# Kernel tuning notes

Hardware: AMD Instinct MI355X
Metric: run time of the kernel (lower is better)

## Reference

```python
import jax, jax.numpy as jnp
import numpy as np

T, B, D, H = 512, 64, 1024, 1024


def setup_inputs() -> dict:
    key = jax.random.key(0)
    ks = jax.random.split(key, 6)
    s_in = 0.02  # small init so tanh/sigmoid don't saturate
    return {
        "x": jax.random.normal(ks[0], (T, B, D), jnp.float32),
        "Wih": jax.random.normal(ks[1], (D, 4 * H), jnp.float32) * s_in,
        "Whh": jax.random.normal(ks[2], (H, 4 * H), jnp.float32) * s_in,
        "b": jnp.zeros((4 * H,), jnp.float32),
        "Wih_r": jax.random.normal(ks[3], (D, 4 * H), jnp.float32) * s_in,
        "Whh_r": jax.random.normal(ks[4], (H, 4 * H), jnp.float32) * s_in,
        "b_r": jnp.zeros((4 * H,), jnp.float32),
    }


def _lstm_scan(x, Wih, Whh, b):
    """Run an LSTM over time-major x [T,B,D]; returns (hs [T,B,H], h_T, c_T)."""
    Bsz = x.shape[1]
    h0 = jnp.zeros((Bsz, H), x.dtype)
    c0 = jnp.zeros((Bsz, H), x.dtype)

    # Precompute input projections for all timesteps in one big GEMM.
    xg = jnp.einsum("tbd,dg->tbg", x, Wih) + b  # [T,B,4H]

    def step(carry, xg_t):
        h, c = carry
        gates = xg_t + h @ Whh  # [B,4H]
        i, f, g, o = jnp.split(gates, 4, axis=-1)
        c_next = jax.nn.sigmoid(f) * c + jax.nn.sigmoid(i) * jnp.tanh(g)
        h_next = jax.nn.sigmoid(o) * jnp.tanh(c_next)
        return (h_next, c_next), h_next

    (hT, cT), hs = jax.lax.scan(step, (h0, c0), xg)
    return hs, hT, cT


def reference(x, Wih, Whh, b, Wih_r, Whh_r, b_r):
    # forward direction
    hs_f, hT, cT = _lstm_scan(x, Wih, Whh, b)
    # backward direction: flip time, run, flip outputs back
    hs_b, _, _ = _lstm_scan(x[::-1], Wih_r, Whh_r, b_r)
    output = jnp.concatenate([hs_f, hs_b[::-1]], axis=-1)  # [T,B,2H]
    # original returns (output, h_n) where h_n is the forward cell's final (h, c)
    return output, hT, cT
```

## Files before the change

### kernel.cpp

```cpp
#include <hip/hip_runtime.h>
#include <hip/hip_bf16.h>


#define TS    512
#define BATCH 64
#define DDIM  1024
#define HDIM  1024
#define KD    2048
#define GD    4096
#define OUT_HS ((size_t)TS * BATCH * 2 * HDIM)
#define HT_OFF OUT_HS
#define CT_OFF (OUT_HS + (size_t)BATCH * HDIM)

#define WP_BYTES   ((size_t)2 * GD * KD * 2)
#define XBF_BYTES  ((size_t)TS * BATCH * DDIM * 2)
#define HS_BYTES   ((size_t)2 * 2 * BATCH * HDIM * 2)
#define BAR_BYTES  ((size_t)4096)
#define WS_A_TOTAL (WP_BYTES + XBF_BYTES + HS_BYTES + BAR_BYTES)
#define WS_B_TOTAL (WP_BYTES + HS_BYTES + BAR_BYTES)

typedef __attribute__((ext_vector_type(8))) short frag8;
typedef __attribute__((ext_vector_type(4))) float f32x4;
typedef unsigned long long u64;

__device__ __forceinline__ ushort f2b(float f) {
  union { float f; unsigned u; } v; v.f = f;
  unsigned r = v.u + 0x7FFFu + ((v.u >> 16) & 1u);
  return (ushort)(r >> 16);
}
__device__ __forceinline__ float sigf(float x) { return 1.0f / (1.0f + __expf(-x)); }
__device__ __forceinline__ float tanh_fast(float x) {
  x = fminf(15.0f, fmaxf(-15.0f, x));
  float e = __expf(2.0f * x);
  return (e - 1.0f) / (e + 1.0f);
}


__global__ void xconv(const float* __restrict__ x, ushort* __restrict__ o) {
  size_t i = ((size_t)blockIdx.x * 256 + threadIdx.x) * 8;
  float4 a = *(const float4*)(x + i);
  float4 b = *(const float4*)(x + i + 4);
  union { ushort s[8]; uint4 v; } r;
  r.s[0] = f2b(a.x); r.s[1] = f2b(a.y); r.s[2] = f2b(a.z); r.s[3] = f2b(a.w);
  r.s[4] = f2b(b.x); r.s[5] = f2b(b.y); r.s[6] = f2b(b.z); r.s[7] = f2b(b.w);
  *(uint4*)(o + i) = r.v;
}

__global__ void wpackk(const float* __restrict__ Wih,  const float* __restrict__ Whh,
                       const float* __restrict__ WihR, const float* __restrict__ WhhR,
                       ushort* __restrict__ wp) {
  __shared__ ushort tile[32][36];
  int bid = blockIdx.x;
  int kt  = bid & 63;
  int pt  = (bid >> 6) & 127;
  int dir = bid >> 13;
  const float* Wi = dir ? WihR : Wih;
  const float* Wh = dir ? WhhR : Whh;
  int t  = threadIdx.x;
  int kl = t >> 3;
  int g  = (t >> 1) & 3;
  int q  = t & 1;
  int k  = kt * 32 + kl;
  const float* srow = (k < 1024) ? (Wi + (size_t)k * GD) : (Wh + (size_t)(k - 1024) * GD);
  float4 v = *(const float4*)(srow + g * 1024 + pt * 8 + q * 4);
  int pl = g * 8 + q * 4;
  tile[kl][pl + 0] = f2b(v.x); tile[kl][pl + 1] = f2b(v.y);
  tile[kl][pl + 2] = f2b(v.z); tile[kl][pl + 3] = f2b(v.w);
  __syncthreads();
  int po = t >> 3;
  int kc = t & 7;
  ushort* dst = wp + ((size_t)dir * GD + pt * 32 + po) * KD + kt * 32 + kc * 4;
  ushort4 ov;
  ov.x = tile[kc * 4 + 0][po]; ov.y = tile[kc * 4 + 1][po];
  ov.z = tile[kc * 4 + 2][po]; ov.w = tile[kc * 4 + 3][po];
  *(ushort4*)dst = ov;
}

#define MFMA(a, b, c) __builtin_amdgcn_mfma_f32_16x16x32_bf16((a), (b), (c), 0, 0, 0)
#define ALOADU64(p) __hip_atomic_load((p), __ATOMIC_RELAXED, __HIP_MEMORY_SCOPE_AGENT)

template <int MODEA>
__global__ __launch_bounds__(256, 1)
void lstm_scan(const ushort* __restrict__ xbf, const float* __restrict__ xf,
               const ushort* __restrict__ wpack,
               const float* __restrict__ bfwd, const float* __restrict__ bbwd,
               ushort* hstate, float* __restrict__ out, unsigned* bar) {
  __shared__ ushort wlds[32 * KD];

  const int tid  = threadIdx.x;
  const int lane = tid & 63;
  const int wv   = tid >> 6;
  const int wg   = blockIdx.x;
  const int dir  = wg >> 7;
  const int wq   = wg & 127;
  unsigned* grpflags = bar + (dir * 4 + wv) * 128;

  {
    const ushort* src = wpack + ((size_t)dir * GD + wq * 32) * KD;
#pragma unroll
    for (int it = 0; it < 32; ++it) {
      int m  = it * 256 + tid;
      int p  = m >> 8;
      int kc = m & 255;
      uint4 v = *(const uint4*)(src + (size_t)p * KD + kc * 8);
      int off = p * 4096 + ((kc * 16) ^ ((p & 7) << 4));
      *(uint4*)((char*)wlds + off) = v;
    }
  }
  __syncthreads();

  const int lm   = lane & 15;
  const int jj   = lane & 7;
  const int kb   = (lane >> 4) * 8;
  const int kb2  = kb * 2;
  const int arow = wv * 16 + lm;
  const int hcol = wq * 8 + jj;
  const int sw   = jj << 4;
  const int b0base = lm * 4096;
  const int b1base = (16 + lm) * 4096;

  const float* bsrc = dir ? bbwd : bfwd;
  const float bias0 = bsrc[(lm >> 3) * HDIM + hcol];
  const float bias1 = bsrc[(2 + (lm >> 3)) * HDIM + hcol];

  float creg[4] = {0.f, 0.f, 0.f, 0.f};
  f32x4 a0a, a0b, a1a, a1b;

  auto compute_x = [&](int tt) {
    const int tsrc = dir ? (TS - 1 - tt) : tt;
    a0a = (f32x4){0.f,0.f,0.f,0.f}; a0b = (f32x4){0.f,0.f,0.f,0.f};
    a1a = (f32x4){0.f,0.f,0.f,0.f}; a1b = (f32x4){0.f,0.f,0.f,0.f};
    if (MODEA) {
      const ushort* xs = xbf + ((size_t)tsrc * BATCH + arow) * DDIM + kb;
#pragma unroll 8
      for (int kk = 0; kk < 32; kk += 2) {
        frag8 a  = *(const frag8*)(xs + kk * 32);
        frag8 a2 = *(const frag8*)(xs + (kk + 1) * 32);
        int ko  = (kk * 64 + kb2) ^ sw;
        int ko2 = ((kk + 1) * 64 + kb2) ^ sw;
        frag8 b0  = *(const frag8*)((const char*)wlds + (b0base + ko));
        frag8 b1  = *(const frag8*)((const char*)wlds + (b1base + ko));
        frag8 b02 = *(const frag8*)((const char*)wlds + (b0base + ko2));
        frag8 b12 = *(const frag8*)((const char*)wlds + (b1base + ko2));
        a0a = MFMA(a, b0, a0a);  a1a = MFMA(a, b1, a1a);
        a0b = MFMA(a2, b02, a0b); a1b = MFMA(a2, b12, a1b);
      }
    } else {
      const float* xs = xf + ((size_t)tsrc * BATCH + arow) * DDIM + kb;
#pragma unroll 4
      for (int kk = 0; kk < 32; ++kk) {
        float4 f0 = *(const float4*)(xs + kk * 32);
        float4 f1 = *(const float4*)(xs + kk * 32 + 4);
        union { ushort s[8]; frag8 fr; } ua;
        ua.s[0] = f2b(f0.x); ua.s[1] = f2b(f0.y); ua.s[2] = f2b(f0.z); ua.s[3] = f2b(f0.w);
        ua.s[4] = f2b(f1.x); ua.s[5] = f2b(f1.y); ua.s[6] = f2b(f1.z); ua.s[7] = f2b(f1.w);
        int ko = (kk * 64 + kb2) ^ sw;
        frag8 b0 = *(const frag8*)((const char*)wlds + (b0base + ko));
        frag8 b1 = *(const frag8*)((const char*)wlds + (b1base + ko));
        if (kk & 1) { a0b = MFMA(ua.fr, b0, a0b); a1b = MFMA(ua.fr, b1, a1b); }
        else        { a0a = MFMA(ua.fr, b0, a0a); a1a = MFMA(ua.fr, b1, a1a); }
      }
    }
  };

  auto h_part = [&](int t) {
    const ushort* hsrd = hstate + (((size_t)(t & 1) * 2 + dir) * BATCH + arow) * HDIM + kb;
    frag8 hf[32];
#pragma unroll
    for (int kk = 0; kk < 32; ++kk)
      asm volatile("global_load_dwordx4 %0, %1, off offset:%2 sc1"
                   : "=v"(hf[kk]) : "v"(hsrd), "i"(kk * 64) : "memory");
    asm volatile("s_waitcnt vmcnt(0)" ::: "memory");
    __builtin_amdgcn_sched_barrier(0);
#pragma unroll
    for (int kk = 0; kk < 32; kk += 2) {
      int ko  = (2048 + kk * 64 + kb2) ^ sw;
      int ko2 = (2048 + (kk + 1) * 64 + kb2) ^ sw;
      frag8 b0  = *(const frag8*)((const char*)wlds + (b0base + ko));
      frag8 b1  = *(const frag8*)((const char*)wlds + (b1base + ko));
      frag8 b02 = *(const frag8*)((const char*)wlds + (b0base + ko2));
      frag8 b12 = *(const frag8*)((const char*)wlds + (b1base + ko2));
      a0a = MFMA(hf[kk], b0, a0a);      a1a = MFMA(hf[kk], b1, a1a);
      a0b = MFMA(hf[kk + 1], b02, a0b); a1b = MFMA(hf[kk + 1], b12, a1b);
    }
  };

  compute_x(0);

  for (int t = 0; t < TS; ++t) {
    if (t > 0) h_part(t);

    const int tsrc = dir ? (TS - 1 - t) : t;
    f32x4 acc0 = a0a + a0b;
    f32x4 acc1 = a1a + a1b;

    ushort* hnext = hstate + ((size_t)(((t + 1) & 1) * 2 + dir) * BATCH) * HDIM;
    const size_t obase = ((size_t)tsrc * BATCH) * (2 * HDIM) + (size_t)dir * HDIM + hcol;
    const bool last = (t == TS - 1);
    const bool last_f = (dir == 0) && last;

#pragma unroll
    for (int i = 0; i < 4; ++i) {
      float g0 = acc0[i] + bias0;
      float g1 = acc1[i] + bias1;
      float q0 = __shfl_xor(g0, 8);
      float q1 = __shfl_xor(g1, 8);
      if ((lane & 8) == 0) {
        float cn = sigf(q0) * creg[i] + sigf(g0) * tanh_fast(g1);
        creg[i] = cn;
        float hv = sigf(q1) * tanh_fast(cn);
        int brow = wv * 16 + (lane >> 4) * 4 + i;
        out[obase + (size_t)brow * (2 * HDIM)] = hv;
        if (!last)
          __hip_atomic_store(hnext + (size_t)brow * HDIM + hcol, f2b(hv),
                             __ATOMIC_RELAXED, __HIP_MEMORY_SCOPE_AGENT);
        if (last_f) {
          out[HT_OFF + (size_t)brow * HDIM + hcol] = hv;
          out[CT_OFF + (size_t)brow * HDIM + hcol] = cn;
        }
      }
    }

    if (last) break;

    asm volatile("s_waitcnt vmcnt(0)" ::: "memory");
    if (lane == 0)
      __hip_atomic_store(grpflags + wq, (unsigned)(t + 1),
                         __ATOMIC_RELAXED, __HIP_MEMORY_SCOPE_AGENT);

    compute_x(t + 1);

    {
      const unsigned want = (unsigned)(t + 1);
      const u64* f2 = (const u64*)grpflags + lane;
      for (;;) {
        u64 v = ALOADU64(f2);
        if ((unsigned)v >= want && (unsigned)(v >> 32) >= want) break;
        __builtin_amdgcn_s_sleep(1);
      }
    }
    __atomic_signal_fence(__ATOMIC_SEQ_CST);
    asm volatile("" ::: "memory");
  }
}

extern "C" void kernel_launch(void* const* d_in, const int* in_sizes, int n_in,
                              void* d_out, int out_size, void* d_ws, size_t ws_size,
                              hipStream_t stream) {
  const float* x    = (const float*)d_in[0];
  const float* Wih  = (const float*)d_in[1];
  const float* Whh  = (const float*)d_in[2];
  const float* b    = (const float*)d_in[3];
  const float* WihR = (const float*)d_in[4];
  const float* WhhR = (const float*)d_in[5];
  const float* bR   = (const float*)d_in[6];
  float* out = (float*)d_out;
  char* ws = (char*)d_ws;

  if (ws_size < WS_B_TOTAL) return;
  const bool modeA = (ws_size >= WS_A_TOTAL);

  ushort* wp  = (ushort*)(ws);
  ushort* xbf = (ushort*)(ws + WP_BYTES);
  size_t hs_off = modeA ? (WP_BYTES + XBF_BYTES) : WP_BYTES;
  ushort* hs = (ushort*)(ws + hs_off);
  unsigned* bar = (unsigned*)(ws + hs_off + HS_BYTES);

  hipMemsetAsync(ws + hs_off + HS_BYTES, 0, BAR_BYTES, stream);

  wpackk<<<dim3(16384), dim3(256), 0, stream>>>(Wih, Whh, WihR, WhhR, wp);

  if (modeA) {
    xconv<<<dim3(16384), dim3(256), 0, stream>>>(x, xbf);
    lstm_scan<1><<<dim3(256), dim3(256), 0, stream>>>(xbf, x, wp, b, bR, hs, out, bar);
  } else {
    lstm_scan<0><<<dim3(256), dim3(256), 0, stream>>>(nullptr, x, wp, b, bR, hs, out, bar);
  }
}
```

Measured before the change: 4.585 ms.

## Move x-projection MFMAs after barrier poll to overlap with split h loads

In the bf16-input mode, the x-tile loads are issued before the grid-barrier poll, and their MFMAs are deferred until after it. The x MFMAs are then interleaved with the recurrent h loads, which are split into two halves with partial vmcnt waits so the MFMAs on the first half can start while the second half is still loading. The intent is to hide global-load latency on the recurrent critical path. In exchange, the x MFMAs now sit after the barrier and may lengthen each step, and holding 64 fragment registers at once raises register pressure.

```diff
diff --git a/kernel.cpp b/kernel.cpp
--- a/kernel.cpp
+++ b/kernel.cpp
@@ -78,6 +78,7 @@
 
 #define MFMA(a, b, c) __builtin_amdgcn_mfma_f32_16x16x32_bf16((a), (b), (c), 0, 0, 0)
 #define ALOADU64(p) __hip_atomic_load((p), __ATOMIC_RELAXED, __HIP_MEMORY_SCOPE_AGENT)
+#define SB() __builtin_amdgcn_sched_barrier(0)
 
 template <int MODEA>
 __global__ __launch_bounds__(256, 1)
@@ -125,80 +126,105 @@
 
   float creg[4] = {0.f, 0.f, 0.f, 0.f};
   f32x4 a0a, a0b, a1a, a1b;
-
-  auto compute_x = [&](int tt) {
+  frag8 xa[32];
+  frag8 hfA[16];
+  frag8 hfB[16];
+
+  auto xload_issue = [&](int tt) {
     const int tsrc = dir ? (TS - 1 - tt) : tt;
+    const ushort* xs = xbf + ((size_t)tsrc * BATCH + arow) * DDIM + kb;
+#pragma unroll
+    for (int kk = 0; kk < 32; ++kk)
+      asm volatile("global_load_dwordx4 %0, %1, off offset:%2"
+                   : "=v"(xa[kk]) : "v"(xs), "i"(kk * 64) : "memory");
+  };
+
+  auto x_mfma = [&]() {
     a0a = (f32x4){0.f,0.f,0.f,0.f}; a0b = (f32x4){0.f,0.f,0.f,0.f};
     a1a = (f32x4){0.f,0.f,0.f,0.f}; a1b = (f32x4){0.f,0.f,0.f,0.f};
-    if (MODEA) {
-      const ushort* xs = xbf + ((size_t)tsrc * BATCH + arow) * DDIM + kb;
-#pragma unroll 8
-      for (int kk = 0; kk < 32; kk += 2) {
-        frag8 a  = *(const frag8*)(xs + kk * 32);
-        frag8 a2 = *(const frag8*)(xs + (kk + 1) * 32);
-        int ko  = (kk * 64 + kb2) ^ sw;
-        int ko2 = ((kk + 1) * 64 + kb2) ^ sw;
-        frag8 b0  = *(const frag8*)((const char*)wlds + (b0base + ko));
-        frag8 b1  = *(const frag8*)((const char*)wlds + (b1base + ko));
-        frag8 b02 = *(const frag8*)((const char*)wlds + (b0base + ko2));
-        frag8 b12 = *(const frag8*)((const char*)wlds + (b1base + ko2));
-        a0a = MFMA(a, b0, a0a);  a1a = MFMA(a, b1, a1a);
-        a0b = MFMA(a2, b02, a0b); a1b = MFMA(a2, b12, a1b);
-      }
-    } else {
-      const float* xs = xf + ((size_t)tsrc * BATCH + arow) * DDIM + kb;
-#pragma unroll 4
-      for (int kk = 0; kk < 32; ++kk) {
-        float4 f0 = *(const float4*)(xs + kk * 32);
-        float4 f1 = *(const float4*)(xs + kk * 32 + 4);
-        union { ushort s[8]; frag8 fr; } ua;
-        ua.s[0] = f2b(f0.x); ua.s[1] = f2b(f0.y); ua.s[2] = f2b(f0.z); ua.s[3] = f2b(f0.w);
-        ua.s[4] = f2b(f1.x); ua.s[5] = f2b(f1.y); ua.s[6] = f2b(f1.z); ua.s[7] = f2b(f1.w);
-        int ko = (kk * 64 + kb2) ^ sw;
-        frag8 b0 = *(const frag8*)((const char*)wlds + (b0base + ko));
-        frag8 b1 = *(const frag8*)((const char*)wlds + (b1base + ko));
-        if (kk & 1) { a0b = MFMA(ua.fr, b0, a0b); a1b = MFMA(ua.fr, b1, a1b); }
-        else        { a0a = MFMA(ua.fr, b0, a0a); a1a = MFMA(ua.fr, b1, a1a); }
-      }
-    }
-  };
-
-  auto h_part = [&](int t) {
+#pragma unroll
+    for (int kk = 0; kk < 32; kk += 2) {
+      int ko  = (kk * 64 + kb2) ^ sw;
+      int ko2 = ((kk + 1) * 64 + kb2) ^ sw;
+      frag8 b0  = *(const frag8*)((const char*)wlds + (b0base + ko));
+      frag8 b1  = *(const frag8*)((const char*)wlds + (b1base + ko));
+      frag8 b02 = *(const frag8*)((const char*)wlds + (b0base + ko2));
+      frag8 b12 = *(const frag8*)((const char*)wlds + (b1base + ko2));
+      a0a = MFMA(xa[kk], b0, a0a);      a1a = MFMA(xa[kk], b1, a1a);
+      a0b = MFMA(xa[kk + 1], b02, a0b); a1b = MFMA(xa[kk + 1], b12, a1b);
+    }
+  };
+
+  auto hloadA = [&](int t) {
     const ushort* hsrd = hstate + (((size_t)(t & 1) * 2 + dir) * BATCH + arow) * HDIM + kb;
-    frag8 hf[32];
-#pragma unroll
-    for (int kk = 0; kk < 32; ++kk)
+#pragma unroll
+    for (int kk = 0; kk < 16; ++kk)
       asm volatile("global_load_dwordx4 %0, %1, off offset:%2 sc1"
-                   : "=v"(hf[kk]) : "v"(hsrd), "i"(kk * 64) : "memory");
-    asm volatile("s_waitcnt vmcnt(0)" ::: "memory");
-    __builtin_amdgcn_sched_barrier(0);
-#pragma unroll
-    for (int kk = 0; kk < 32; kk += 2) {
+                   : "=v"(hfA[kk]) : "v"(hsrd), "i"(kk * 64) : "memory");
+  };
+  auto hloadB = [&](int t) {
+    const ushort* hsrd = hstate + (((size_t)(t & 1) * 2 + dir) * BATCH + arow) * HDIM + kb;
+#pragma unroll
+    for (int kk = 0; kk < 16; ++kk)
+      asm volatile("global_load_dwordx4 %0, %1, off offset:%2 sc1"
+                   : "=v"(hfB[kk]) : "v"(hsrd), "i"(1024 + kk * 64) : "memory");
+  };
+
+  auto h_mfmaA = [&]() {
+#pragma unroll
+    for (int kk = 0; kk < 16; kk += 2) {
       int ko  = (2048 + kk * 64 + kb2) ^ sw;
       int ko2 = (2048 + (kk + 1) * 64 + kb2) ^ sw;
       frag8 b0  = *(const frag8*)((const char*)wlds + (b0base + ko));
       frag8 b1  = *(const frag8*)((const char*)wlds + (b1base + ko));
       frag8 b02 = *(const frag8*)((const char*)wlds + (b0base + ko2));
       frag8 b12 = *(const frag8*)((const char*)wlds + (b1base + ko2));
-      a0a = MFMA(hf[kk], b0, a0a);      a1a = MFMA(hf[kk], b1, a1a);
-      a0b = MFMA(hf[kk + 1], b02, a0b); a1b = MFMA(hf[kk + 1], b12, a1b);
-    }
-  };
-
-  compute_x(0);
-
-  for (int t = 0; t < TS; ++t) {
-    if (t > 0) h_part(t);
-
+      a0a = MFMA(hfA[kk], b0, a0a);      a1a = MFMA(hfA[kk], b1, a1a);
+      a0b = MFMA(hfA[kk + 1], b02, a0b); a1b = MFMA(hfA[kk + 1], b12, a1b);
+    }
+  };
+  auto h_mfmaB = [&]() {
+#pragma unroll
+    for (int kk = 16; kk < 32; kk += 2) {
+      int ko  = (2048 + kk * 64 + kb2) ^ sw;
+      int ko2 = (2048 + (kk + 1) * 64 + kb2) ^ sw;
+      frag8 b0  = *(const frag8*)((const char*)wlds + (b0base + ko));
+      frag8 b1  = *(const frag8*)((const char*)wlds + (b1base + ko));
+      frag8 b02 = *(const frag8*)((const char*)wlds + (b0base + ko2));
+      frag8 b12 = *(const frag8*)((const char*)wlds + (b1base + ko2));
+      a0a = MFMA(hfB[kk - 16], b0, a0a);      a1a = MFMA(hfB[kk - 16], b1, a1a);
+      a0b = MFMA(hfB[kk - 15], b02, a0b);     a1b = MFMA(hfB[kk - 15], b12, a1b);
+    }
+  };
+
+  auto compute_x_old = [&](int tt) {
+    const int tsrc = dir ? (TS - 1 - tt) : tt;
+    a0a = (f32x4){0.f,0.f,0.f,0.f}; a0b = (f32x4){0.f,0.f,0.f,0.f};
+    a1a = (f32x4){0.f,0.f,0.f,0.f}; a1b = (f32x4){0.f,0.f,0.f,0.f};
+    const float* xs = xf + ((size_t)tsrc * BATCH + arow) * DDIM + kb;
+#pragma unroll 4
+    for (int kk = 0; kk < 32; ++kk) {
+      float4 f0 = *(const float4*)(xs + kk * 32);
+      float4 f1 = *(const float4*)(xs + kk * 32 + 4);
+      union { ushort s[8]; frag8 fr; } ua;
+      ua.s[0] = f2b(f0.x); ua.s[1] = f2b(f0.y); ua.s[2] = f2b(f0.z); ua.s[3] = f2b(f0.w);
+      ua.s[4] = f2b(f1.x); ua.s[5] = f2b(f1.y); ua.s[6] = f2b(f1.z); ua.s[7] = f2b(f1.w);
+      int ko = (kk * 64 + kb2) ^ sw;
+      frag8 b0 = *(const frag8*)((const char*)wlds + (b0base + ko));
+      frag8 b1 = *(const frag8*)((const char*)wlds + (b1base + ko));
+      if (kk & 1) { a0b = MFMA(ua.fr, b0, a0b); a1b = MFMA(ua.fr, b1, a1b); }
+      else        { a0a = MFMA(ua.fr, b0, a0a); a1a = MFMA(ua.fr, b1, a1a); }
+    }
+  };
+
+  auto epilogue = [&](int t) {
     const int tsrc = dir ? (TS - 1 - t) : t;
     f32x4 acc0 = a0a + a0b;
     f32x4 acc1 = a1a + a1b;
-
     ushort* hnext = hstate + ((size_t)(((t + 1) & 1) * 2 + dir) * BATCH) * HDIM;
     const size_t obase = ((size_t)tsrc * BATCH) * (2 * HDIM) + (size_t)dir * HDIM + hcol;
     const bool last = (t == TS - 1);
     const bool last_f = (dir == 0) && last;
-
 #pragma unroll
     for (int i = 0; i < 4; ++i) {
       float g0 = acc0[i] + bias0;
@@ -220,27 +246,65 @@
         }
       }
     }
-
-    if (last) break;
-
+  };
+
+  auto publish = [&](int gen) {
     asm volatile("s_waitcnt vmcnt(0)" ::: "memory");
     if (lane == 0)
-      __hip_atomic_store(grpflags + wq, (unsigned)(t + 1),
+      __hip_atomic_store(grpflags + wq, (unsigned)gen,
                          __ATOMIC_RELAXED, __HIP_MEMORY_SCOPE_AGENT);
-
-    compute_x(t + 1);
-
-    {
-      const unsigned want = (unsigned)(t + 1);
-      const u64* f2 = (const u64*)grpflags + lane;
-      for (;;) {
-        u64 v = ALOADU64(f2);
-        if ((unsigned)v >= want && (unsigned)(v >> 32) >= want) break;
-        __builtin_amdgcn_s_sleep(1);
-      }
+  };
+
+  auto poll = [&](int gen) {
+    const unsigned want = (unsigned)gen;
+    const u64* f2 = (const u64*)grpflags + lane;
+    for (;;) {
+      u64 v = ALOADU64(f2);
+      if ((unsigned)v >= want && (unsigned)(v >> 32) >= want) break;
+      __builtin_amdgcn_s_sleep(1);
     }
     __atomic_signal_fence(__ATOMIC_SEQ_CST);
     asm volatile("" ::: "memory");
+  };
+
+  if (MODEA) {
+    xload_issue(0);
+    asm volatile("s_waitcnt vmcnt(0)" ::: "memory");
+    SB();
+    x_mfma();
+    for (int t = 0; t < TS; ++t) {
+      epilogue(t);
+      if (t == TS - 1) break;
+      publish(t + 1);
+      xload_issue(t + 1);
+      poll(t + 1);
+      SB();
+      hloadA(t + 1);
+      x_mfma();
+      hloadB(t + 1);
+      asm volatile("s_waitcnt vmcnt(16)" ::: "memory");
+      SB();
+      h_mfmaA();
+      asm volatile("s_waitcnt vmcnt(0)" ::: "memory");
+      SB();
+      h_mfmaB();
+    }
+  } else {
+    compute_x_old(0);
+    for (int t = 0; t < TS; ++t) {
+      if (t > 0) {
+        hloadA(t); hloadB(t);
+        asm volatile("s_waitcnt vmcnt(0)" ::: "memory");
+        SB();
+        h_mfmaA(); h_mfmaB();
+      }
+      epilogue(t);
+      if (t == TS - 1) break;
+      publish(t + 1);
+      compute_x_old(t + 1);
+      poll(t + 1);
+      SB();
+    }
   }
 }
 
```

Result: slower. 6.387 ms (+39.3%).
